# Optimization experiments

Measured on AMD Instinct MI355X. Metric: run time of the kernel, lower is better.

## Reference

```python
import jax, jax.numpy as jnp
import numpy as np
import math

B, S, D, H = 2, 2048, 1024, 16
HD = D // H  # head_dim = 64


def setup_inputs() -> dict:
    key = jax.random.key(0)
    k1, k2, k3, k4, k5 = jax.random.split(key, 5)
    scale_in = 1.0 / math.sqrt(D)
    return {
        "x": jax.random.normal(k1, (B, S, D), dtype=jnp.float32),
        "Wqkv": jax.random.normal(k2, (3 * D, D), dtype=jnp.float32) * scale_in,
        "bqkv": jax.random.normal(k3, (3 * D,), dtype=jnp.float32) * 0.01,
        "Wout": jax.random.normal(k4, (D, D), dtype=jnp.float32) * scale_in,
        "bout": jax.random.normal(k5, (D,), dtype=jnp.float32) * 0.01,
    }


def reference(x, Wqkv, bqkv, Wout, bout):
    Bs, Sl, Dm = x.shape
    # qkv projection: torch Linear is x @ W.T + b
    qkv = x @ Wqkv.T + bqkv                        # [B,S,3D]
    qkv = qkv.reshape(Bs, Sl, 3, H, HD)
    q, k, v = qkv[:, :, 0], qkv[:, :, 1], qkv[:, :, 2]  # each [B,S,H,d]
    softmax_scale = 1.0 / math.sqrt(HD)
    # NOTE: source einsum 'bshd,btjd->bsht' sums k over its head axis j.
    # Equivalent efficient form: pre-sum k (and v) over heads.
    k_sum = k.sum(axis=2)                          # [B,S,d]
    v_sum = v.sum(axis=2)                          # [B,S,d]
    scores = jnp.einsum('bshd,btd->bsht', q, k_sum) * softmax_scale  # [B,S,H,T]
    causal_mask = jnp.triu(jnp.ones((Sl, Sl), dtype=bool), k=1)      # [S,T]
    scores = jnp.where(causal_mask[None, :, None, :], -jnp.inf, scores)
    attn = jax.nn.softmax(scores, axis=-1)
    # dropout p=0.0 / eval mode -> identity
    out = jnp.einsum('bsht,btd->bshd', attn, v_sum)  # [B,S,H,d]
    out = out.reshape(Bs, Sl, Dm)
    return out @ Wout.T + bout
```

## Files before the change

### kernel.cpp

```cpp
#include <hip/hip_runtime.h>


#define S_LEN 2048
#define DIM 1024

using floatx4 = __attribute__((ext_vector_type(4))) float;
using halfx8  = __attribute__((ext_vector_type(8))) _Float16;
using halfx4  = __attribute__((ext_vector_type(4))) _Float16;

__device__ __forceinline__ floatx4 mfma16(halfx8 a, halfx8 b, floatx4 c) {
  return __builtin_amdgcn_mfma_f32_16x16x32_f16(a, b, c, 0, 0, 0);
}

__device__ __forceinline__ void gll16(const void* g, void* l) {
  __builtin_amdgcn_global_load_lds(
      (const __attribute__((address_space(1))) void*)g,
      (__attribute__((address_space(3))) void*)l, 16, 0, 0);
}

__global__ __launch_bounds__(256) void prep_all(
    const float* __restrict__ x, const float* __restrict__ wqkv,
    const float* __restrict__ bqkv, const float* __restrict__ wout,
    _Float16* __restrict__ xb, _Float16* __restrict__ wcomb,
    _Float16* __restrict__ woutb, float* __restrict__ bcomb) {
  int bx = blockIdx.x;
  if (bx < 6144) {
    size_t i4 = ((size_t)bx * 256 + threadIdx.x) * 4;
    const float* src;
    _Float16* dst;
    size_t off;
    if (i4 < 4194304) { src = x; dst = xb; off = i4; }
    else if (i4 < 5242880) { src = wqkv; dst = wcomb; off = i4 - 4194304; }
    else { src = wout; dst = woutb; off = i4 - 5242880; }
    float4 v = *(const float4*)(src + off);
    halfx4 o;
    o[0] = (_Float16)v.x; o[1] = (_Float16)v.y;
    o[2] = (_Float16)v.z; o[3] = (_Float16)v.w;
    *(halfx4*)(dst + off) = o;
  } else {
    int gid = (bx - 6144) * 256 + threadIdx.x;
    int c = gid >> 10, j = gid & 1023;
    int row0 = (c < 64) ? (1024 + c) : (2048 + c - 64);
    float s = 0.f;
#pragma unroll
    for (int h = 0; h < 16; ++h) s += wqkv[(size_t)(row0 + h * 64) * 1024 + j];
    wcomb[(size_t)1024 * 1024 + gid] = (_Float16)s;
    if (gid < 1024) bcomb[gid] = bqkv[gid];
    if (gid < 128) {
      int b0 = (gid < 64) ? (1024 + gid) : (2048 + gid - 64);
      float sb = 0.f;
#pragma unroll
      for (int h = 0; h < 16; ++h) sb += bqkv[b0 + h * 64];
      bcomb[1024 + gid] = sb;
    }
  }
}

template <int MODE>
__global__ __launch_bounds__(256, 2) void gemm_t2(
    const _Float16* __restrict__ A, const _Float16* __restrict__ W,
    const float* __restrict__ bias, void* __restrict__ Cv,
    _Float16* __restrict__ kbo, _Float16* __restrict__ vto) {
  const int K = 1024;
  __shared__ _Float16 As[128][64];
  __shared__ _Float16 Ws[128][64];
  int tid = threadIdx.x;
  int lane = tid & 63, w = tid >> 6, ln = lane & 15, q4 = lane >> 4;
  int m0 = blockIdx.x * 128, n0 = blockIdx.y * 128;
  int mh = (w & 1) * 64, nh = (w >> 1) * 64;
  int rr = lane >> 3, gg = ((lane & 7) ^ rr) * 8;
  const _Float16* agp = A + (size_t)(m0 + w * 32 + rr) * K + gg;
  const _Float16* wgp = W + (size_t)(n0 + w * 32 + rr) * K + gg;
  floatx4 acc[4][4] = {};
  for (int kt = 0; kt < K; kt += 64) {
    __syncthreads();
#pragma unroll
    for (int j = 0; j < 4; ++j) {
      gll16(agp + (size_t)(8 * j) * K + kt, &As[w * 32 + 8 * j][0]);
      gll16(wgp + (size_t)(8 * j) * K + kt, &Ws[w * 32 + 8 * j][0]);
    }
    __syncthreads();
#pragma unroll
    for (int kh = 0; kh < 2; ++kh) {
      int sw = ((q4 + 4 * kh) ^ (ln & 7)) * 8;
      halfx8 bf[4];
#pragma unroll
      for (int nf = 0; nf < 4; ++nf)
        bf[nf] = *(const halfx8*)&Ws[nh + nf * 16 + ln][sw];
#pragma unroll
      for (int mf = 0; mf < 4; ++mf) {
        halfx8 af = *(const halfx8*)&As[mh + mf * 16 + ln][sw];
#pragma unroll
        for (int nf = 0; nf < 4; ++nf)
          acc[mf][nf] = mfma16(af, bf[nf], acc[mf][nf]);
      }
    }
  }
  const float qscale = 0.18033688011112042f;
#pragma unroll
  for (int nf = 0; nf < 4; ++nf) {
    int col = n0 + nh + nf * 16 + ln;
    float bv = bias[col];
    if constexpr (MODE == 1) {
#pragma unroll
      for (int mf = 0; mf < 4; ++mf)
#pragma unroll
        for (int i = 0; i < 4; ++i) {
          int row = m0 + mh + mf * 16 + q4 * 4 + i;
          ((float*)Cv)[(size_t)row * 1024 + col] = acc[mf][nf][i] + bv;
        }
    } else {
      if (col < 1024) {
#pragma unroll
        for (int mf = 0; mf < 4; ++mf)
#pragma unroll
          for (int i = 0; i < 4; ++i) {
            int row = m0 + mh + mf * 16 + q4 * 4 + i;
            ((_Float16*)Cv)[(size_t)row * 1024 + col] =
                (_Float16)((acc[mf][nf][i] + bv) * qscale);
          }
      } else if (col < 1088) {
        int ck = col - 1024;
#pragma unroll
        for (int mf = 0; mf < 4; ++mf)
#pragma unroll
          for (int i = 0; i < 4; ++i) {
            int row = m0 + mh + mf * 16 + q4 * 4 + i;
            kbo[(size_t)row * 64 + ck] = (_Float16)(acc[mf][nf][i] + bv);
          }
      } else {
        int d = col - 1088;
#pragma unroll
        for (int mf = 0; mf < 4; ++mf) {
          int row0 = m0 + mh + mf * 16 + q4 * 4;
          int bb = row0 >> 11, sps = row0 & 2047;
          halfx4 o;
#pragma unroll
          for (int i = 0; i < 4; ++i) o[i] = (_Float16)(acc[mf][nf][i] + bv);
          *(halfx4*)&vto[((size_t)((bb << 6) + d)) * S_LEN + sps] = o;
        }
      }
    }
  }
}

__global__ __launch_bounds__(256, 4) void flash_attn7(
    const _Float16* __restrict__ Qb, const _Float16* __restrict__ kb,
    const _Float16* __restrict__ vtb, _Float16* __restrict__ aob) {
  __shared__ _Float16 Ks[128][64];
  __shared__ _Float16 Vt[64][128];
  __shared__ _Float16 Ps[4][16][72];
  int tid = threadIdx.x;
  int lane = tid & 63, w = tid >> 6, ln = lane & 15, q4 = lane >> 4;
  int idx = 1023 - (int)blockIdx.x;
  int c = idx >> 1, b = idx & 1;
  int s0 = c * 4;
  int s = s0 + w;
  size_t bS = (size_t)b * S_LEN;

  const _Float16* qp = Qb + (bS + s) * DIM + ln * 64 + q4 * 8;
  halfx8 bq0 = *(const halfx8*)qp, bq1 = *(const halfx8*)(qp + 32);

  float m_run = -1e30f, l_run = 0.f;
  floatx4 oacc[4] = {};

  int rr = lane >> 3, ggk = ((lane & 7) ^ rr) * 8;
  const _Float16* kgp = kb + (bS + w * 32 + rr) * 64 + ggk;
  int vrow = (lane >> 4);
  int vhalf = (lane >> 3) & 1, vg = lane & 7;
  const _Float16* vgp[4];
#pragma unroll
  for (int j = 0; j < 4; ++j) {
    int row = w * 16 + 4 * j + vrow;
    vgp[j] = vtb + ((size_t)b * 64 + row) * S_LEN + vhalf * 64 +
             ((vg ^ (row & 7)) * 8);
  }
  int swk0 = (q4 ^ (ln & 7)) * 8;
  int swk1 = ((q4 + 4) ^ (ln & 7)) * 8;
  _Float16* Pw = &Ps[w][0][0];
  int nt = (s0 >> 7) + 1;

  for (int it = 0; it < nt; ++it) {
    int t0 = it << 7;
    __syncthreads();
#pragma unroll
    for (int j = 0; j < 4; ++j) {
      gll16(kgp + (size_t)(t0 + 8 * j) * 64, &Ks[w * 32 + 8 * j][0]);
      gll16(vgp[j] + t0, &Vt[w * 16 + 4 * j][0]);
    }
    __syncthreads();

#pragma unroll
    for (int tq = 0; tq < 2; ++tq) {
      int t0q = t0 + tq * 64;
      if (t0q > s) break;
      floatx4 sf[4];
#pragma unroll
      for (int tf = 0; tf < 4; ++tf) {
        halfx8 ak0 = *(const halfx8*)&Ks[tq * 64 + tf * 16 + ln][swk0];
        halfx8 ak1 = *(const halfx8*)&Ks[tq * 64 + tf * 16 + ln][swk1];
        floatx4 z = {};
        z = mfma16(ak0, bq0, z);
        sf[tf] = mfma16(ak1, bq1, z);
      }
      if (t0q + 63 > s) {
#pragma unroll
        for (int tf = 0; tf < 4; ++tf)
#pragma unroll
          for (int i = 0; i < 4; ++i) {
            int t = t0q + tf * 16 + q4 * 4 + i;
            if (t > s) sf[tf][i] = -1e30f;
          }
      }
      float tm = fmaxf(fmaxf(sf[0][0], sf[0][1]), fmaxf(sf[0][2], sf[0][3]));
#pragma unroll
      for (int tf = 1; tf < 4; ++tf)
        tm = fmaxf(tm, fmaxf(fmaxf(sf[tf][0], sf[tf][1]),
                             fmaxf(sf[tf][2], sf[tf][3])));
      tm = fmaxf(tm, __shfl_xor(tm, 16));
      tm = fmaxf(tm, __shfl_xor(tm, 32));
      float mn = fmaxf(m_run, tm);
      float alpha = exp2f(m_run - mn);
      m_run = mn;
      float rs = 0.f;
#pragma unroll
      for (int tf = 0; tf < 4; ++tf) {
        float p0 = exp2f(sf[tf][0] - mn), p1 = exp2f(sf[tf][1] - mn);
        float p2 = exp2f(sf[tf][2] - mn), p3 = exp2f(sf[tf][3] - mn);
        rs += (p0 + p1) + (p2 + p3);
        halfx4 pk;
        pk[0] = (_Float16)p0; pk[1] = (_Float16)p1;
        pk[2] = (_Float16)p2; pk[3] = (_Float16)p3;
        *(halfx4*)&Pw[ln * 72 + tf * 16 + q4 * 4] = pk;
      }
      rs += __shfl_xor(rs, 16);
      rs += __shfl_xor(rs, 32);
      l_run = l_run * alpha + rs;
      halfx8 bp0 = *(const halfx8*)&Pw[ln * 72 + q4 * 8];
      halfx8 bp1 = *(const halfx8*)&Pw[ln * 72 + 32 + q4 * 8];
#pragma unroll
      for (int n2 = 0; n2 < 4; ++n2) {
        halfx8 av0 = *(const halfx8*)&Vt[n2 * 16 + ln][tq * 64 + swk0];
        halfx8 av1 = *(const halfx8*)&Vt[n2 * 16 + ln][tq * 64 + swk1];
#pragma unroll
        for (int i = 0; i < 4; ++i) oacc[n2][i] *= alpha;
        oacc[n2] = mfma16(av0, bp0, oacc[n2]);
        oacc[n2] = mfma16(av1, bp1, oacc[n2]);
      }
    }
  }
  float inv = 1.0f / l_run;
#pragma unroll
  for (int n2 = 0; n2 < 4; ++n2) {
    halfx4 o;
#pragma unroll
    for (int i = 0; i < 4; ++i) o[i] = (_Float16)(oacc[n2][i] * inv);
    *(halfx4*)(aob + (bS + s) * DIM + ln * 64 + n2 * 16 + q4 * 4) = o;
  }
}

extern "C" void kernel_launch(void* const* d_in, const int* in_sizes, int n_in,
                              void* d_out, int out_size, void* d_ws,
                              size_t ws_size, hipStream_t stream) {
  const float* x    = (const float*)d_in[0];
  const float* wqkv = (const float*)d_in[1];
  const float* bqkv = (const float*)d_in[2];
  const float* wout = (const float*)d_in[3];
  const float* bout = (const float*)d_in[4];
  float* out = (float*)d_out;
  char* ws = (char*)d_ws;
  _Float16* xb    = (_Float16*)(ws);
  _Float16* qb    = (_Float16*)(ws + (8u << 20));
  _Float16* aob   = (_Float16*)(ws + (16u << 20));
  _Float16* kb    = (_Float16*)(ws + (24u << 20));
  _Float16* vtb   = (_Float16*)(ws + (24u << 20) + (512u << 10));
  _Float16* wcomb = (_Float16*)(ws + (25u << 20));
  _Float16* woutb = (_Float16*)(ws + (27u << 20) + (512u << 10));
  float*    bcomb = (float*)(ws + (29u << 20) + (512u << 10));

  hipLaunchKernelGGL(prep_all, dim3(6656), dim3(256), 0, stream,
                     x, wqkv, bqkv, wout, xb, wcomb, woutb, bcomb);
  hipLaunchKernelGGL((gemm_t2<0>), dim3(32, 9), dim3(256), 0, stream,
                     xb, wcomb, bcomb, (void*)qb, kb, vtb);
  hipLaunchKernelGGL(flash_attn7, dim3(1024), dim3(256), 0, stream,
                     qb, kb, vtb, aob);
  hipLaunchKernelGGL((gemm_t2<1>), dim3(32, 8), dim3(256), 0, stream,
                     aob, woutb, bout, (void*)out, nullptr, nullptr);
}
```

Measured before the change: 169.4 us.

## Split-K both GEMMs with atomic fp32 accumulation and separate convert pass

Both projection GEMMs now split K into two halves along a grid z dimension and accumulate into fp32 buffers with atomicAdd. Those buffers are zeroed or bias-prefilled in the prep kernel, and a new conversion kernel applies bias, q scaling and the V transpose. The aim is to double the block count and fill more CUs than the 256-288 block grids did. The cost is extra fp32 traffic, per-element atomics, one more launch, and nondeterministic summation order. The softmax probability packing also switches to the cvt_pkrtz builtin.

```diff
diff --git a/kernel.cpp b/kernel.cpp
--- a/kernel.cpp
+++ b/kernel.cpp
@@ -7,6 +7,7 @@
 using floatx4 = __attribute__((ext_vector_type(4))) float;
 using halfx8  = __attribute__((ext_vector_type(8))) _Float16;
 using halfx4  = __attribute__((ext_vector_type(4))) _Float16;
+using fp16x2  = __attribute__((ext_vector_type(2))) __fp16;
 
 __device__ __forceinline__ floatx4 mfma16(halfx8 a, halfx8 b, floatx4 c) {
   return __builtin_amdgcn_mfma_f32_16x16x32_f16(a, b, c, 0, 0, 0);
@@ -21,8 +22,10 @@
 __global__ __launch_bounds__(256) void prep_all(
     const float* __restrict__ x, const float* __restrict__ wqkv,
     const float* __restrict__ bqkv, const float* __restrict__ wout,
-    _Float16* __restrict__ xb, _Float16* __restrict__ wcomb,
-    _Float16* __restrict__ woutb, float* __restrict__ bcomb) {
+    const float* __restrict__ bout, _Float16* __restrict__ xb,
+    _Float16* __restrict__ wcomb, _Float16* __restrict__ woutb,
+    float* __restrict__ bcomb, float* __restrict__ qf,
+    float* __restrict__ outp) {
   int bx = blockIdx.x;
   if (bx < 6144) {
     size_t i4 = ((size_t)bx * 256 + threadIdx.x) * 4;
@@ -37,7 +40,7 @@
     o[0] = (_Float16)v.x; o[1] = (_Float16)v.y;
     o[2] = (_Float16)v.z; o[3] = (_Float16)v.w;
     *(halfx4*)(dst + off) = o;
-  } else {
+  } else if (bx < 6656) {
     int gid = (bx - 6144) * 256 + threadIdx.x;
     int c = gid >> 10, j = gid & 1023;
     int row0 = (c < 64) ? (1024 + c) : (2048 + c - 64);
@@ -53,26 +56,33 @@
       for (int h = 0; h < 16; ++h) sb += bqkv[b0 + h * 64];
       bcomb[1024 + gid] = sb;
     }
-  }
-}
-
-template <int MODE>
-__global__ __launch_bounds__(256, 2) void gemm_t2(
+  } else if (bx < 11264) {
+    size_t i4 = ((size_t)(bx - 6656) * 256 + threadIdx.x) * 4;
+    float4 z = {0.f, 0.f, 0.f, 0.f};
+    *(float4*)(qf + i4) = z;
+  } else {
+    size_t i4 = ((size_t)(bx - 11264) * 256 + threadIdx.x) * 4;
+    int col = (int)(i4 & 1023);
+    *(float4*)(outp + i4) = *(const float4*)(bout + col);
+  }
+}
+
+__global__ __launch_bounds__(256, 2) void gemm_sk(
     const _Float16* __restrict__ A, const _Float16* __restrict__ W,
-    const float* __restrict__ bias, void* __restrict__ Cv,
-    _Float16* __restrict__ kbo, _Float16* __restrict__ vto) {
+    float* __restrict__ C, int ldc) {
   const int K = 1024;
   __shared__ _Float16 As[128][64];
   __shared__ _Float16 Ws[128][64];
   int tid = threadIdx.x;
   int lane = tid & 63, w = tid >> 6, ln = lane & 15, q4 = lane >> 4;
   int m0 = blockIdx.x * 128, n0 = blockIdx.y * 128;
+  int kb0 = blockIdx.z * 512;
   int mh = (w & 1) * 64, nh = (w >> 1) * 64;
   int rr = lane >> 3, gg = ((lane & 7) ^ rr) * 8;
-  const _Float16* agp = A + (size_t)(m0 + w * 32 + rr) * K + gg;
-  const _Float16* wgp = W + (size_t)(n0 + w * 32 + rr) * K + gg;
+  const _Float16* agp = A + (size_t)(m0 + w * 32 + rr) * K + kb0 + gg;
+  const _Float16* wgp = W + (size_t)(n0 + w * 32 + rr) * K + kb0 + gg;
   floatx4 acc[4][4] = {};
-  for (int kt = 0; kt < K; kt += 64) {
+  for (int kt = 0; kt < 512; kt += 64) {
     __syncthreads();
 #pragma unroll
     for (int j = 0; j < 4; ++j) {
@@ -96,50 +106,54 @@
       }
     }
   }
-  const float qscale = 0.18033688011112042f;
 #pragma unroll
   for (int nf = 0; nf < 4; ++nf) {
     int col = n0 + nh + nf * 16 + ln;
-    float bv = bias[col];
-    if constexpr (MODE == 1) {
-#pragma unroll
-      for (int mf = 0; mf < 4; ++mf)
-#pragma unroll
-        for (int i = 0; i < 4; ++i) {
-          int row = m0 + mh + mf * 16 + q4 * 4 + i;
-          ((float*)Cv)[(size_t)row * 1024 + col] = acc[mf][nf][i] + bv;
-        }
+#pragma unroll
+    for (int mf = 0; mf < 4; ++mf) {
+      int row = m0 + mh + mf * 16 + q4 * 4;
+#pragma unroll
+      for (int i = 0; i < 4; ++i)
+        atomicAdd(&C[(size_t)(row + i) * ldc + col], acc[mf][nf][i]);
+    }
+  }
+}
+
+__global__ __launch_bounds__(256) void qkv_convert(
+    const float* __restrict__ qf, const float* __restrict__ bcomb,
+    _Float16* __restrict__ qb, _Float16* __restrict__ kbo,
+    _Float16* __restrict__ vto) {
+  const float qscale = 0.18033688011112042f;
+  int bx = blockIdx.x;
+  if (bx < 4096) {
+    size_t gid = (size_t)bx * 256 + threadIdx.x;
+    int row = (int)(gid >> 8), col = ((int)gid & 255) * 4;
+    float4 v = *(const float4*)(qf + (size_t)row * 1152 + col);
+    float4 bv = *(const float4*)(bcomb + col);
+    halfx4 o;
+    o[0] = (_Float16)((v.x + bv.x) * qscale);
+    o[1] = (_Float16)((v.y + bv.y) * qscale);
+    o[2] = (_Float16)((v.z + bv.z) * qscale);
+    o[3] = (_Float16)((v.w + bv.w) * qscale);
+    *(halfx4*)(qb + (size_t)row * 1024 + col) = o;
+  } else {
+    int gid = (bx - 4096) * 256 + threadIdx.x;
+    int row = gid >> 5, c = (gid & 31) * 4;
+    float4 v = *(const float4*)(qf + (size_t)row * 1152 + 1024 + c);
+    float4 bv = *(const float4*)(bcomb + 1024 + c);
+    float r0 = v.x + bv.x, r1 = v.y + bv.y, r2 = v.z + bv.z, r3 = v.w + bv.w;
+    if (c < 64) {
+      halfx4 o;
+      o[0] = (_Float16)r0; o[1] = (_Float16)r1;
+      o[2] = (_Float16)r2; o[3] = (_Float16)r3;
+      *(halfx4*)(kbo + (size_t)row * 64 + c) = o;
     } else {
-      if (col < 1024) {
-#pragma unroll
-        for (int mf = 0; mf < 4; ++mf)
-#pragma unroll
-          for (int i = 0; i < 4; ++i) {
-            int row = m0 + mh + mf * 16 + q4 * 4 + i;
-            ((_Float16*)Cv)[(size_t)row * 1024 + col] =
-                (_Float16)((acc[mf][nf][i] + bv) * qscale);
-          }
-      } else if (col < 1088) {
-        int ck = col - 1024;
-#pragma unroll
-        for (int mf = 0; mf < 4; ++mf)
-#pragma unroll
-          for (int i = 0; i < 4; ++i) {
-            int row = m0 + mh + mf * 16 + q4 * 4 + i;
-            kbo[(size_t)row * 64 + ck] = (_Float16)(acc[mf][nf][i] + bv);
-          }
-      } else {
-        int d = col - 1088;
-#pragma unroll
-        for (int mf = 0; mf < 4; ++mf) {
-          int row0 = m0 + mh + mf * 16 + q4 * 4;
-          int bb = row0 >> 11, sps = row0 & 2047;
-          halfx4 o;
-#pragma unroll
-          for (int i = 0; i < 4; ++i) o[i] = (_Float16)(acc[mf][nf][i] + bv);
-          *(halfx4*)&vto[((size_t)((bb << 6) + d)) * S_LEN + sps] = o;
-        }
-      }
+      int bb = row >> 11, s = row & 2047;
+      int d = c - 64;
+      vto[((size_t)((bb << 6) + d + 0)) * S_LEN + s] = (_Float16)r0;
+      vto[((size_t)((bb << 6) + d + 1)) * S_LEN + s] = (_Float16)r1;
+      vto[((size_t)((bb << 6) + d + 2)) * S_LEN + s] = (_Float16)r2;
+      vto[((size_t)((bb << 6) + d + 3)) * S_LEN + s] = (_Float16)r3;
     }
   }
 }
@@ -228,10 +242,10 @@
         float p0 = exp2f(sf[tf][0] - mn), p1 = exp2f(sf[tf][1] - mn);
         float p2 = exp2f(sf[tf][2] - mn), p3 = exp2f(sf[tf][3] - mn);
         rs += (p0 + p1) + (p2 + p3);
-        halfx4 pk;
-        pk[0] = (_Float16)p0; pk[1] = (_Float16)p1;
-        pk[2] = (_Float16)p2; pk[3] = (_Float16)p3;
-        *(halfx4*)&Pw[ln * 72 + tf * 16 + q4 * 4] = pk;
+        union { fp16x2 h2[2]; halfx4 h4; } u;
+        u.h2[0] = __builtin_amdgcn_cvt_pkrtz(p0, p1);
+        u.h2[1] = __builtin_amdgcn_cvt_pkrtz(p2, p3);
+        *(halfx4*)&Pw[ln * 72 + tf * 16 + q4 * 4] = u.h4;
       }
       rs += __shfl_xor(rs, 16);
       rs += __shfl_xor(rs, 32);
@@ -270,20 +284,24 @@
   float* out = (float*)d_out;
   char* ws = (char*)d_ws;
   _Float16* xb    = (_Float16*)(ws);
+  _Float16* aob   = (_Float16*)(ws);
   _Float16* qb    = (_Float16*)(ws + (8u << 20));
-  _Float16* aob   = (_Float16*)(ws + (16u << 20));
-  _Float16* kb    = (_Float16*)(ws + (24u << 20));
-  _Float16* vtb   = (_Float16*)(ws + (24u << 20) + (512u << 10));
-  _Float16* wcomb = (_Float16*)(ws + (25u << 20));
-  _Float16* woutb = (_Float16*)(ws + (27u << 20) + (512u << 10));
-  float*    bcomb = (float*)(ws + (29u << 20) + (512u << 10));
-
-  hipLaunchKernelGGL(prep_all, dim3(6656), dim3(256), 0, stream,
-                     x, wqkv, bqkv, wout, xb, wcomb, woutb, bcomb);
-  hipLaunchKernelGGL((gemm_t2<0>), dim3(32, 9), dim3(256), 0, stream,
-                     xb, wcomb, bcomb, (void*)qb, kb, vtb);
+  float*    qf    = (float*)(ws + (16u << 20));
+  _Float16* kb    = (_Float16*)(ws + (35u << 20));
+  _Float16* vtb   = (_Float16*)(ws + (35u << 20) + (512u << 10));
+  _Float16* wcomb = (_Float16*)(ws + (36u << 20));
+  _Float16* woutb = (_Float16*)(ws + (38u << 20) + (512u << 10));
+  float*    bcomb = (float*)(ws + (40u << 20) + (512u << 10));
+
+  hipLaunchKernelGGL(prep_all, dim3(15360), dim3(256), 0, stream,
+                     x, wqkv, bqkv, wout, bout, xb, wcomb, woutb, bcomb, qf,
+                     out);
+  hipLaunchKernelGGL(gemm_sk, dim3(32, 9, 2), dim3(256), 0, stream,
+                     xb, wcomb, qf, 1152);
+  hipLaunchKernelGGL(qkv_convert, dim3(4608), dim3(256), 0, stream,
+                     qf, bcomb, qb, kb, vtb);
   hipLaunchKernelGGL(flash_attn7, dim3(1024), dim3(256), 0, stream,
                      qb, kb, vtb, aob);
-  hipLaunchKernelGGL((gemm_t2<1>), dim3(32, 8), dim3(256), 0, stream,
-                     aob, woutb, bout, (void*)out, nullptr, nullptr);
-}
+  hipLaunchKernelGGL(gemm_sk, dim3(32, 8, 2), dim3(256), 0, stream,
+                     aob, woutb, out, 1024);
+}
```

Measured after the change: 212.4 us. 25.4% more time.
